# Performance work log

Measured on AMD Instinct MI355X. Metric: run time of the kernel, lower is better.

Reference implementation:

```python
import jax, jax.numpy as jnp
import numpy as np

N_NODES = 20000
N_EDGES = 640000
IN_DIM, HIDDEN, OUT_DIM = 128, 256, 64
EPS = 1e-12


def setup_inputs() -> dict:
    key = jax.random.key(0)
    ks = jax.random.split(key, 8)
    x = jax.random.normal(ks[0], (N_NODES, IN_DIM), dtype=jnp.float32)
    edge_src = jax.random.randint(ks[1], (N_EDGES,), 0, N_NODES, dtype=jnp.int32)
    edge_dst = jax.random.randint(ks[2], (N_EDGES,), 0, N_NODES, dtype=jnp.int32)
    s1 = 1.0 / np.sqrt(IN_DIM)
    s2 = 1.0 / np.sqrt(HIDDEN)
    W1 = jax.random.uniform(ks[3], (IN_DIM, HIDDEN), jnp.float32, -s1, s1)
    b1 = jax.random.uniform(ks[4], (HIDDEN,), jnp.float32, -s1, s1)
    W2 = jax.random.uniform(ks[5], (HIDDEN, OUT_DIM), jnp.float32, -s2, s2)
    b2 = jax.random.uniform(ks[6], (OUT_DIM,), jnp.float32, -s2, s2)
    return {"x": x, "edge_src": edge_src, "edge_dst": edge_dst,
            "W1": W1, "b1": b1, "W2": W2, "b2": b2}


def _agnn_layer(h, src, dst, n_nodes):
    # AGNN propagation with beta = 1 (non-trainable buffer in source module):
    # out_i = sum_j softmax_j(cos(h_i, h_j)) * h_j over neighbors j (incl. self-loop)
    hn = h * jax.lax.rsqrt(jnp.sum(h * h, axis=-1, keepdims=True) + EPS)
    logits = jnp.sum(hn[src] * hn[dst], axis=-1)            # [E] cosine similarity
    m = jax.ops.segment_max(logits, dst, num_segments=n_nodes)
    e = jnp.exp(logits - m[dst])
    z = jax.ops.segment_sum(e, dst, num_segments=n_nodes)
    alpha = e / z[dst]                                       # per-dst softmax
    return jax.ops.segment_sum(alpha[:, None] * h[src], dst, num_segments=n_nodes)


def reference(x, edge_src, edge_dst, W1, b1, W2, b2):
    n = x.shape[0]
    loop = jnp.arange(n, dtype=edge_src.dtype)
    src = jnp.concatenate([edge_src, loop])
    dst = jnp.concatenate([edge_dst, loop])
    h = jax.nn.relu(x @ W1 + b1)
    for _ in range(4):
        h = jax.nn.relu(_agnn_layer(h, src, dst, n))
    return h @ W2 + b2
```

## Files before the change

kernel.cpp:

```cpp
#include <hip/hip_runtime.h>

#define N_NODES 20000
#define N_EDGES 640000
#define E_TOT   (N_EDGES + N_NODES)
#define IN_DIM  128
#define HIDDEN  256
#define OUT_DIM 64
#define LOG2E 1.4426950408889634f
#define NSHARD 8

typedef __attribute__((ext_vector_type(2))) float f32x2;

__device__ __forceinline__ unsigned short f2bf(float f) {
    union { float f; unsigned int i; } x; x.f = f;
    unsigned int u = x.i;
    return (unsigned short)((u + 0x7fffu + ((u >> 16) & 1u)) >> 16);
}
__device__ __forceinline__ f32x2 up2(unsigned int p) {
    f32x2 r;
    r.x = __uint_as_float(p << 16);
    r.y = __uint_as_float(p & 0xffff0000u);
    return r;
}
__device__ __forceinline__ unsigned int pk2(float a, float b) {
    return (unsigned int)f2bf(a) | ((unsigned int)f2bf(b) << 16);
}


__global__ void zero_cnt8_kernel(int* __restrict__ cnt8) {
    int i = blockIdx.x * blockDim.x + threadIdx.x;
    if (i < NSHARD * N_NODES) cnt8[i] = 0;
}

__global__ void count_kernel(const int* __restrict__ edge_dst, int* __restrict__ cnt8) {
    int i = blockIdx.x * blockDim.x + threadIdx.x;
    if (i >= E_TOT) return;
    int shard = blockIdx.x & (NSHARD - 1);
    int d = (i < N_EDGES) ? edge_dst[i] : (i - N_EDGES);
    atomicAdd(&cnt8[shard * N_NODES + d], 1);
}

__global__ void sumdeg_kernel(const int* __restrict__ cnt8, int* __restrict__ deg) {
    int i = blockIdx.x * blockDim.x + threadIdx.x;
    if (i >= N_NODES) return;
    int s = 0;
#pragma unroll
    for (int s8 = 0; s8 < NSHARD; s8++) s += cnt8[s8 * N_NODES + i];
    deg[i] = s;
}

__global__ __launch_bounds__(1024) void scan1b_kernel(const int* __restrict__ deg,
                                                      int* __restrict__ indptr) {
    const int T = 1024;
    const int C = (N_NODES + T - 1) / T;
    __shared__ int sums[T];
    int t = threadIdx.x;
    int base = t * C;
    int local[C];
    int s = 0;
#pragma unroll
    for (int i = 0; i < C; i++) {
        int idx = base + i;
        int v = (idx < N_NODES) ? deg[idx] : 0;
        local[i] = s;
        s += v;
    }
    sums[t] = s;
    __syncthreads();
    for (int off = 1; off < T; off <<= 1) {
        int v = (t >= off) ? sums[t - off] : 0;
        __syncthreads();
        sums[t] += v;
        __syncthreads();
    }
    int prefix = (t == 0) ? 0 : sums[t - 1];
#pragma unroll
    for (int i = 0; i < C; i++) {
        int idx = base + i;
        if (idx < N_NODES) indptr[idx] = prefix + local[i];
    }
    if (t == T - 1) indptr[N_NODES] = prefix + s;
}

__global__ void cursor_kernel(const int* __restrict__ indptr, int* __restrict__ cnt8) {
    int i = blockIdx.x * blockDim.x + threadIdx.x;
    if (i >= N_NODES) return;
    int running = indptr[i];
#pragma unroll
    for (int s8 = 0; s8 < NSHARD; s8++) {
        int c = cnt8[s8 * N_NODES + i];
        cnt8[s8 * N_NODES + i] = running;
        running += c;
    }
}

__global__ void scatter_edges_kernel(const int* __restrict__ edge_src,
                                     const int* __restrict__ edge_dst,
                                     int* __restrict__ cnt8,
                                     int* __restrict__ ssrc) {
    int i = blockIdx.x * blockDim.x + threadIdx.x;
    if (i >= E_TOT) return;
    int shard = blockIdx.x & (NSHARD - 1);
    int d, s;
    if (i < N_EDGES) { d = edge_dst[i]; s = edge_src[i]; }
    else             { d = i - N_EDGES; s = d; }
    int pos = atomicAdd(&cnt8[shard * N_NODES + d], 1);
    ssrc[pos] = s;
}


__global__ __launch_bounds__(256) void gemm1_norm_kernel(const float* __restrict__ A,
                                                         const float* __restrict__ W,
                                                         const float* __restrict__ bias,
                                                         unsigned short* __restrict__ hnb,
                                                         float* __restrict__ r) {
    __shared__ float As[16][20];
    __shared__ float Bs[16][260];
    int t = threadIdx.x;
    int row = t >> 4;
    int cg  = t & 15;
    int grow = blockIdx.x * 16 + row;
    float4 acc0 = make_float4(0.f, 0.f, 0.f, 0.f);
    float4 acc1 = acc0, acc2 = acc0, acc3 = acc0;

    for (int k0 = 0; k0 < IN_DIM; k0 += 16) {
        {
            As[row][cg] = A[(long)grow * IN_DIM + k0 + cg];
        }
        {
            const float4* src = (const float4*)&W[(long)(k0 + row) * HIDDEN];
#pragma unroll
            for (int j = 0; j < 4; j++)
                *((float4*)&Bs[row][4 * cg + 64 * j]) = src[cg + 16 * j];
        }
        __syncthreads();
#pragma unroll
        for (int kk = 0; kk < 16; kk++) {
            float a = As[row][kk];
            float4 q0 = *((const float4*)&Bs[kk][4 * cg]);
            float4 q1 = *((const float4*)&Bs[kk][4 * cg + 64]);
            float4 q2 = *((const float4*)&Bs[kk][4 * cg + 128]);
            float4 q3 = *((const float4*)&Bs[kk][4 * cg + 192]);
            acc0.x += a * q0.x; acc0.y += a * q0.y; acc0.z += a * q0.z; acc0.w += a * q0.w;
            acc1.x += a * q1.x; acc1.y += a * q1.y; acc1.z += a * q1.z; acc1.w += a * q1.w;
            acc2.x += a * q2.x; acc2.y += a * q2.y; acc2.z += a * q2.z; acc2.w += a * q2.w;
            acc3.x += a * q3.x; acc3.y += a * q3.y; acc3.z += a * q3.z; acc3.w += a * q3.w;
        }
        __syncthreads();
    }

    float ss = 0.f;
    {
        float4 bv = *((const float4*)&bias[4 * cg]);
        acc0.x = fmaxf(acc0.x + bv.x, 0.f); acc0.y = fmaxf(acc0.y + bv.y, 0.f);
        acc0.z = fmaxf(acc0.z + bv.z, 0.f); acc0.w = fmaxf(acc0.w + bv.w, 0.f);
        ss += acc0.x * acc0.x + acc0.y * acc0.y + acc0.z * acc0.z + acc0.w * acc0.w;
    }
    {
        float4 bv = *((const float4*)&bias[4 * cg + 64]);
        acc1.x = fmaxf(acc1.x + bv.x, 0.f); acc1.y = fmaxf(acc1.y + bv.y, 0.f);
        acc1.z = fmaxf(acc1.z + bv.z, 0.f); acc1.w = fmaxf(acc1.w + bv.w, 0.f);
        ss += acc1.x * acc1.x + acc1.y * acc1.y + acc1.z * acc1.z + acc1.w * acc1.w;
    }
    {
        float4 bv = *((const float4*)&bias[4 * cg + 128]);
        acc2.x = fmaxf(acc2.x + bv.x, 0.f); acc2.y = fmaxf(acc2.y + bv.y, 0.f);
        acc2.z = fmaxf(acc2.z + bv.z, 0.f); acc2.w = fmaxf(acc2.w + bv.w, 0.f);
        ss += acc2.x * acc2.x + acc2.y * acc2.y + acc2.z * acc2.z + acc2.w * acc2.w;
    }
    {
        float4 bv = *((const float4*)&bias[4 * cg + 192]);
        acc3.x = fmaxf(acc3.x + bv.x, 0.f); acc3.y = fmaxf(acc3.y + bv.y, 0.f);
        acc3.z = fmaxf(acc3.z + bv.z, 0.f); acc3.w = fmaxf(acc3.w + bv.w, 0.f);
        ss += acc3.x * acc3.x + acc3.y * acc3.y + acc3.z * acc3.z + acc3.w * acc3.w;
    }
    ss += __shfl_xor(ss, 1);
    ss += __shfl_xor(ss, 2);
    ss += __shfl_xor(ss, 4);
    ss += __shfl_xor(ss, 8);
    float rr = sqrtf(ss + 1e-12f);
    float ir = 1.f / rr;
    uint2* dst = (uint2*)(hnb + (long)grow * HIDDEN);
    uint2 o;
    o.x = pk2(acc0.x * ir, acc0.y * ir); o.y = pk2(acc0.z * ir, acc0.w * ir);
    dst[cg]      = o;
    o.x = pk2(acc1.x * ir, acc1.y * ir); o.y = pk2(acc1.z * ir, acc1.w * ir);
    dst[cg + 16] = o;
    o.x = pk2(acc2.x * ir, acc2.y * ir); o.y = pk2(acc2.z * ir, acc2.w * ir);
    dst[cg + 32] = o;
    o.x = pk2(acc3.x * ir, acc3.y * ir); o.y = pk2(acc3.z * ir, acc3.w * ir);
    dst[cg + 48] = o;
    if (cg == 0) r[grow] = rr;
}


__global__ __launch_bounds__(256) void gemm_bias_act(const float* __restrict__ A,
                                                     const float* __restrict__ B,
                                                     const float* __restrict__ bias,
                                                     float* __restrict__ C,
                                                     int M, int Nn, int K, int relu) {
    __shared__ float As[16][65];
    __shared__ float Bs[16][65];
    int tid = threadIdx.x;
    int tx = tid & 15, ty = tid >> 4;
    int row0 = blockIdx.x * 64, col0 = blockIdx.y * 64;
    float acc[4][4] = {};
    for (int k0 = 0; k0 < K; k0 += 16) {
        {
            int r_ = tid >> 2;
            int kq = (tid & 3) * 4;
            int gr = row0 + r_;
            float4 a4 = make_float4(0.f, 0.f, 0.f, 0.f);
            if (gr < M) a4 = *(const float4*)&A[(long)gr * K + k0 + kq];
            As[kq + 0][r_] = a4.x; As[kq + 1][r_] = a4.y;
            As[kq + 2][r_] = a4.z; As[kq + 3][r_] = a4.w;
        }
        {
            int kr = tid >> 4;
            int cq = (tid & 15) * 4;
            float4 b4 = *(const float4*)&B[(long)(k0 + kr) * Nn + col0 + cq];
            Bs[kr][cq + 0] = b4.x; Bs[kr][cq + 1] = b4.y;
            Bs[kr][cq + 2] = b4.z; Bs[kr][cq + 3] = b4.w;
        }
        __syncthreads();
#pragma unroll
        for (int kk = 0; kk < 16; kk++) {
            float a[4], b[4];
#pragma unroll
            for (int i = 0; i < 4; i++) a[i] = As[kk][ty * 4 + i];
#pragma unroll
            for (int j = 0; j < 4; j++) b[j] = Bs[kk][tx * 4 + j];
#pragma unroll
            for (int i = 0; i < 4; i++)
#pragma unroll
                for (int j = 0; j < 4; j++) acc[i][j] += a[i] * b[j];
        }
        __syncthreads();
    }
#pragma unroll
    for (int i = 0; i < 4; i++) {
        int gr = row0 + ty * 4 + i;
        if (gr >= M) continue;
#pragma unroll
        for (int j = 0; j < 4; j++) {
            int gc = col0 + tx * 4 + j;
            float v = acc[i][j] + bias[gc];
            if (relu) v = fmaxf(v, 0.f);
            C[(long)gr * Nn + gc] = v;
        }
    }
}


__global__ __launch_bounds__(256) void agnn_kernel(const unsigned short* __restrict__ hnb,
                                                   const float* __restrict__ rin,
                                                   const int* __restrict__ indptr,
                                                   const int* __restrict__ ssrc,
                                                   unsigned short* __restrict__ hnout,
                                                   float* __restrict__ rout,
                                                   float* __restrict__ hout,
                                                   int write_hn) {
    int lane = threadIdx.x & 63;
    int wid  = threadIdx.x >> 6;
    int sub  = lane >> 4;
    int gl   = lane & 15;
    int node = blockIdx.x * 4 + wid;

    const uint4* tab4 = (const uint4*)hnb;
    long nb = (long)node * 32 + gl * 2;
    uint4 ha = tab4[nb], hb = tab4[nb + 1];
    f32x2 hd2[8];
    hd2[0] = up2(ha.x) * LOG2E; hd2[1] = up2(ha.y) * LOG2E;
    hd2[2] = up2(ha.z) * LOG2E; hd2[3] = up2(ha.w) * LOG2E;
    hd2[4] = up2(hb.x) * LOG2E; hd2[5] = up2(hb.y) * LOG2E;
    hd2[6] = up2(hb.z) * LOG2E; hd2[7] = up2(hb.w) * LOG2E;

    int beg = indptr[node], end = indptr[node + 1];
    int deg = end - beg;
    int qb  = deg >> 2, rem = deg & 3;
    int cnt = qb + (sub < rem ? 1 : 0);
    int eb  = beg + sub * qb + min(sub, rem);
    int nmax = qb + (rem ? 1 : 0);

    f32x2 acc[8];
#pragma unroll
    for (int p = 0; p < 8; p++) acc[p] = (f32x2)0.f;
    float z = 0.f;

    int s0 = ssrc[(cnt > 0) ? eb : beg];
    long b0 = (long)s0 * 32 + gl * 2;
    uint4 v0a = tab4[b0], v0b = tab4[b0 + 1];
    float r0 = rin[s0];
    uint4 v1a = v0a, v1b = v0b;
    float r1 = 0.f;
    int s2 = s0;
    if (cnt >= 2) {
        int s1 = ssrc[eb + 1];
        long b1 = (long)s1 * 32 + gl * 2;
        v1a = tab4[b1]; v1b = tab4[b1 + 1];
        r1 = rin[s1];
    }
    if (cnt >= 3) s2 = ssrc[eb + 2];

    for (int i = 0; i < nmax; i++) {
        uint4 ca = v0a, cb = v0b;
        float cr = r0;
        v0a = v1a; v0b = v1b; r0 = r1;
        if (i + 2 < cnt) {
            long b2 = (long)s2 * 32 + gl * 2;
            v1a = tab4[b2]; v1b = tab4[b2 + 1];
            r1 = rin[s2];
        }
        if (i + 3 < cnt) s2 = ssrc[eb + i + 3];

        f32x2 cf[8];
        cf[0] = up2(ca.x); cf[1] = up2(ca.y); cf[2] = up2(ca.z); cf[3] = up2(ca.w);
        cf[4] = up2(cb.x); cf[5] = up2(cb.y); cf[6] = up2(cb.z); cf[7] = up2(cb.w);
        f32x2 da = cf[0] * hd2[0];
        f32x2 db = cf[1] * hd2[1];
        da += cf[2] * hd2[2];  db += cf[3] * hd2[3];
        da += cf[4] * hd2[4];  db += cf[5] * hd2[5];
        da += cf[6] * hd2[6];  db += cf[7] * hd2[7];
        f32x2 d2 = da + db;
        float d = d2.x + d2.y;
        d += __shfl_xor(d, 1);
        d += __shfl_xor(d, 2);
        d += __shfl_xor(d, 4);
        d += __shfl_xor(d, 8);
        float w = (i < cnt) ? exp2f(d) : 0.f;
        z += w;
        float wr = w * cr;
#pragma unroll
        for (int p = 0; p < 8; p++) acc[p] += cf[p] * wr;
    }

    z += __shfl_xor(z, 16);
    z += __shfl_xor(z, 32);
#pragma unroll
    for (int p = 0; p < 8; p++) {
        acc[p].x += __shfl_xor(acc[p].x, 16);
        acc[p].y += __shfl_xor(acc[p].y, 16);
        acc[p].x += __shfl_xor(acc[p].x, 32);
        acc[p].y += __shfl_xor(acc[p].y, 32);
    }

    float inv = 1.f / z;
    f32x2 o[8];
#pragma unroll
    for (int p = 0; p < 8; p++) {
        f32x2 t = acc[p] * inv;
        t.x = fmaxf(t.x, 0.f);
        t.y = fmaxf(t.y, 0.f);
        o[p] = t;
    }

    if (write_hn) {
        float ss = 0.f;
#pragma unroll
        for (int p = 0; p < 8; p++) ss += o[p].x * o[p].x + o[p].y * o[p].y;
        ss += __shfl_xor(ss, 1);
        ss += __shfl_xor(ss, 2);
        ss += __shfl_xor(ss, 4);
        ss += __shfl_xor(ss, 8);
        float rr = sqrtf(ss + 1e-12f);
        float ir = 1.f / rr;
        if (sub == 0) {
            uint4 oa, ob;
            oa.x = pk2(o[0].x * ir, o[0].y * ir);
            oa.y = pk2(o[1].x * ir, o[1].y * ir);
            oa.z = pk2(o[2].x * ir, o[2].y * ir);
            oa.w = pk2(o[3].x * ir, o[3].y * ir);
            ob.x = pk2(o[4].x * ir, o[4].y * ir);
            ob.y = pk2(o[5].x * ir, o[5].y * ir);
            ob.z = pk2(o[6].x * ir, o[6].y * ir);
            ob.w = pk2(o[7].x * ir, o[7].y * ir);
            uint4* outt = (uint4*)hnout;
            outt[nb] = oa;
            outt[nb + 1] = ob;
            if (gl == 0) rout[node] = rr;
        }
    } else {
        if (sub == 0) {
            float4* ho = (float4*)(hout + (long)node * HIDDEN + gl * 16);
            ho[0] = make_float4(o[0].x, o[0].y, o[1].x, o[1].y);
            ho[1] = make_float4(o[2].x, o[2].y, o[3].x, o[3].y);
            ho[2] = make_float4(o[4].x, o[4].y, o[5].x, o[5].y);
            ho[3] = make_float4(o[6].x, o[6].y, o[7].x, o[7].y);
        }
    }
}


extern "C" void kernel_launch(void* const* d_in, const int* in_sizes, int n_in,
                              void* d_out, int out_size, void* d_ws, size_t ws_size,
                              hipStream_t stream) {
    const float* x  = (const float*)d_in[0];
    const int* esrc = (const int*)d_in[1];
    const int* edst = (const int*)d_in[2];
    const float* W1 = (const float*)d_in[3];
    const float* b1 = (const float*)d_in[4];
    const float* W2 = (const float*)d_in[5];
    const float* b2 = (const float*)d_in[6];
    float* out = (float*)d_out;

    char* ws = (char*)d_ws;
    float*          h0     = (float*)(ws);
    unsigned short* hnA    = (unsigned short*)(ws + 20480000);
    unsigned short* hnB    = (unsigned short*)(ws + 30720000);
    float*          rA     = (float*)(ws + 40960000);
    float*          rB     = (float*)(ws + 41040000);
    int*            indptr = (int*)  (ws + 41120000);
    int*            cnt8   = (int*)  (ws + 41200256);
    int*            ssrc   = (int*)  (ws + 41840256);
    int*            deg    = (int*)  (ws + 44480256);

    zero_cnt8_kernel<<<(NSHARD * N_NODES + 255) / 256, 256, 0, stream>>>(cnt8);
    count_kernel<<<(E_TOT + 255) / 256, 256, 0, stream>>>(edst, cnt8);
    sumdeg_kernel<<<(N_NODES + 255) / 256, 256, 0, stream>>>(cnt8, deg);
    scan1b_kernel<<<1, 1024, 0, stream>>>(deg, indptr);
    cursor_kernel<<<(N_NODES + 255) / 256, 256, 0, stream>>>(indptr, cnt8);
    scatter_edges_kernel<<<(E_TOT + 255) / 256, 256, 0, stream>>>(esrc, edst, cnt8, ssrc);

    gemm1_norm_kernel<<<N_NODES / 16, 256, 0, stream>>>(x, W1, b1, hnA, rA);

    int nblk = N_NODES / 4;
    agnn_kernel<<<nblk, 256, 0, stream>>>(hnA, rA, indptr, ssrc, hnB, rB, h0, 1);
    agnn_kernel<<<nblk, 256, 0, stream>>>(hnB, rB, indptr, ssrc, hnA, rA, h0, 1);
    agnn_kernel<<<nblk, 256, 0, stream>>>(hnA, rA, indptr, ssrc, hnB, rB, h0, 1);
    agnn_kernel<<<nblk, 256, 0, stream>>>(hnB, rB, indptr, ssrc, hnA, rA, h0, 0);

    dim3 g2((N_NODES + 63) / 64, OUT_DIM / 64);
    gemm_bias_act<<<g2, 256, 0, stream>>>(h0, W2, b2, out, N_NODES, OUT_DIM, HIDDEN, 0);
}
```

Baseline: 309.9 us.

## Fuse CSR construction kernels into one cooperative kernel with grid syncs

Replaces the six separate CSR-building launches (zero, count, degree sum, scan, cursor, scatter) with a single cooperative kernel that separates the phases with grid-wide syncs. The single-block scan is replaced by a two-level wave-shuffle scan over 1000 chunks of 20 nodes. This is meant to remove per-launch overhead and the serial single-block scan. In exchange it adds grid.sync costs and caps parallelism at 1024 blocks for the edge loops, and it requires all 1024 blocks to be co-resident.

```diff
diff --git a/kernel.cpp b/kernel.cpp
--- a/kernel.cpp
+++ b/kernel.cpp
@@ -1,4 +1,7 @@
 #include <hip/hip_runtime.h>
+#include <hip/hip_cooperative_groups.h>
+
+namespace cg = cooperative_groups;
 
 #define N_NODES 20000
 #define N_EDGES 640000
@@ -8,6 +11,8 @@
 #define OUT_DIM 64
 #define LOG2E 1.4426950408889634f
 #define NSHARD 8
+#define CSR_BLOCKS 1024
+#define CSR_THREADS 256
 
 typedef __attribute__((ext_vector_type(2))) float f32x2;
 
@@ -27,85 +32,108 @@
 }
 
 
-__global__ void zero_cnt8_kernel(int* __restrict__ cnt8) {
-    int i = blockIdx.x * blockDim.x + threadIdx.x;
-    if (i < NSHARD * N_NODES) cnt8[i] = 0;
-}
-
-__global__ void count_kernel(const int* __restrict__ edge_dst, int* __restrict__ cnt8) {
-    int i = blockIdx.x * blockDim.x + threadIdx.x;
-    if (i >= E_TOT) return;
-    int shard = blockIdx.x & (NSHARD - 1);
-    int d = (i < N_EDGES) ? edge_dst[i] : (i - N_EDGES);
-    atomicAdd(&cnt8[shard * N_NODES + d], 1);
-}
-
-__global__ void sumdeg_kernel(const int* __restrict__ cnt8, int* __restrict__ deg) {
-    int i = blockIdx.x * blockDim.x + threadIdx.x;
-    if (i >= N_NODES) return;
-    int s = 0;
-#pragma unroll
-    for (int s8 = 0; s8 < NSHARD; s8++) s += cnt8[s8 * N_NODES + i];
-    deg[i] = s;
-}
-
-__global__ __launch_bounds__(1024) void scan1b_kernel(const int* __restrict__ deg,
-                                                      int* __restrict__ indptr) {
-    const int T = 1024;
-    const int C = (N_NODES + T - 1) / T;
-    __shared__ int sums[T];
-    int t = threadIdx.x;
-    int base = t * C;
-    int local[C];
-    int s = 0;
-#pragma unroll
-    for (int i = 0; i < C; i++) {
-        int idx = base + i;
-        int v = (idx < N_NODES) ? deg[idx] : 0;
-        local[i] = s;
-        s += v;
-    }
-    sums[t] = s;
-    __syncthreads();
-    for (int off = 1; off < T; off <<= 1) {
-        int v = (t >= off) ? sums[t - off] : 0;
+__global__ __launch_bounds__(CSR_THREADS) void csr_coop_kernel(
+        const int* __restrict__ esrc, const int* __restrict__ edst,
+        int* __restrict__ cnt8, int* __restrict__ deg, int* __restrict__ indptr,
+        int* __restrict__ bsum, int* __restrict__ ssrc) {
+    cg::grid_group grid = cg::this_grid();
+    int bid = blockIdx.x, tid = threadIdx.x;
+    int gtid = bid * CSR_THREADS + tid;
+    const int GT = CSR_BLOCKS * CSR_THREADS;
+    int shard = bid & (NSHARD - 1);
+
+    for (int i = gtid; i < NSHARD * N_NODES; i += GT) cnt8[i] = 0;
+    grid.sync();
+
+    for (int i = gtid; i < E_TOT; i += GT) {
+        int d = (i < N_EDGES) ? edst[i] : (i - N_EDGES);
+        atomicAdd(&cnt8[shard * N_NODES + d], 1);
+    }
+    grid.sync();
+
+    for (int i = gtid; i < N_NODES; i += GT) {
+        int s = 0;
+#pragma unroll
+        for (int s8 = 0; s8 < NSHARD; s8++) s += cnt8[s8 * N_NODES + i];
+        deg[i] = s;
+    }
+    grid.sync();
+
+    if (bid < 1000 && tid < 32) {
+        int idx = bid * 20 + tid;
+        int v = (tid < 20) ? deg[idx] : 0;
+        int x = v;
+#pragma unroll
+        for (int off = 1; off < 32; off <<= 1) {
+            int y = __shfl_up(x, off);
+            if (tid >= off) x += y;
+        }
+        if (tid == 19) bsum[bid] = x;
+    }
+    grid.sync();
+
+    if (bid == 0) {
+        __shared__ int sm[CSR_THREADS];
+        int base = tid * 4;
+        int l0 = 0, l1 = 0, l2 = 0, l3 = 0;
+        if (base < 1000) {
+            l0 = bsum[base];
+            l1 = (base + 1 < 1000) ? bsum[base + 1] : 0;
+            l2 = (base + 2 < 1000) ? bsum[base + 2] : 0;
+            l3 = (base + 3 < 1000) ? bsum[base + 3] : 0;
+        }
+        int tot = l0 + l1 + l2 + l3;
+        sm[tid] = tot;
         __syncthreads();
-        sums[t] += v;
-        __syncthreads();
-    }
-    int prefix = (t == 0) ? 0 : sums[t - 1];
-#pragma unroll
-    for (int i = 0; i < C; i++) {
-        int idx = base + i;
-        if (idx < N_NODES) indptr[idx] = prefix + local[i];
-    }
-    if (t == T - 1) indptr[N_NODES] = prefix + s;
-}
-
-__global__ void cursor_kernel(const int* __restrict__ indptr, int* __restrict__ cnt8) {
-    int i = blockIdx.x * blockDim.x + threadIdx.x;
-    if (i >= N_NODES) return;
-    int running = indptr[i];
-#pragma unroll
-    for (int s8 = 0; s8 < NSHARD; s8++) {
-        int c = cnt8[s8 * N_NODES + i];
-        cnt8[s8 * N_NODES + i] = running;
-        running += c;
-    }
-}
-
-__global__ void scatter_edges_kernel(const int* __restrict__ edge_src,
-                                     const int* __restrict__ edge_dst,
-                                     int* __restrict__ cnt8,
-                                     int* __restrict__ ssrc) {
-    int i = blockIdx.x * blockDim.x + threadIdx.x;
-    if (i >= E_TOT) return;
-    int shard = blockIdx.x & (NSHARD - 1);
-    int d, s;
-    if (i < N_EDGES) { d = edge_dst[i]; s = edge_src[i]; }
-    else             { d = i - N_EDGES; s = d; }
-    int pos = atomicAdd(&cnt8[shard * N_NODES + d], 1);
-    ssrc[pos] = s;
+        for (int off = 1; off < CSR_THREADS; off <<= 1) {
+            int v = (tid >= off) ? sm[tid - off] : 0;
+            __syncthreads();
+            sm[tid] += v;
+            __syncthreads();
+        }
+        int pre = (tid == 0) ? 0 : sm[tid - 1];
+        if (base < 1000) {
+            bsum[base] = pre;
+            if (base + 1 < 1000) bsum[base + 1] = pre + l0;
+            if (base + 2 < 1000) bsum[base + 2] = pre + l0 + l1;
+            if (base + 3 < 1000) bsum[base + 3] = pre + l0 + l1 + l2;
+        }
+        if (tid == CSR_THREADS - 1) bsum[1000] = sm[CSR_THREADS - 1];
+    }
+    grid.sync();
+
+    if (bid < 1000 && tid < 32) {
+        int idx = bid * 20 + tid;
+        int v = (tid < 20) ? deg[idx] : 0;
+        int x = v;
+#pragma unroll
+        for (int off = 1; off < 32; off <<= 1) {
+            int y = __shfl_up(x, off);
+            if (tid >= off) x += y;
+        }
+        if (tid < 20) indptr[idx] = bsum[bid] + x - v;
+    }
+    if (gtid == 0) indptr[N_NODES] = bsum[1000];
+    grid.sync();
+
+    for (int i = gtid; i < N_NODES; i += GT) {
+        int running = indptr[i];
+#pragma unroll
+        for (int s8 = 0; s8 < NSHARD; s8++) {
+            int c = cnt8[s8 * N_NODES + i];
+            cnt8[s8 * N_NODES + i] = running;
+            running += c;
+        }
+    }
+    grid.sync();
+
+    for (int i = gtid; i < E_TOT; i += GT) {
+        int d, s;
+        if (i < N_EDGES) { d = edst[i]; s = esrc[i]; }
+        else             { d = i - N_EDGES; s = d; }
+        int pos = atomicAdd(&cnt8[shard * N_NODES + d], 1);
+        ssrc[pos] = s;
+    }
 }
 
 
@@ -124,9 +152,7 @@
     float4 acc1 = acc0, acc2 = acc0, acc3 = acc0;
 
     for (int k0 = 0; k0 < IN_DIM; k0 += 16) {
-        {
-            As[row][cg] = A[(long)grow * IN_DIM + k0 + cg];
-        }
+        As[row][cg] = A[(long)grow * IN_DIM + k0 + cg];
         {
             const float4* src = (const float4*)&W[(long)(k0 + row) * HIDDEN];
 #pragma unroll
@@ -413,13 +439,15 @@
     int*            cnt8   = (int*)  (ws + 41200256);
     int*            ssrc   = (int*)  (ws + 41840256);
     int*            deg    = (int*)  (ws + 44480256);
-
-    zero_cnt8_kernel<<<(NSHARD * N_NODES + 255) / 256, 256, 0, stream>>>(cnt8);
-    count_kernel<<<(E_TOT + 255) / 256, 256, 0, stream>>>(edst, cnt8);
-    sumdeg_kernel<<<(N_NODES + 255) / 256, 256, 0, stream>>>(cnt8, deg);
-    scan1b_kernel<<<1, 1024, 0, stream>>>(deg, indptr);
-    cursor_kernel<<<(N_NODES + 255) / 256, 256, 0, stream>>>(indptr, cnt8);
-    scatter_edges_kernel<<<(E_TOT + 255) / 256, 256, 0, stream>>>(esrc, edst, cnt8, ssrc);
+    int*            bsum   = (int*)  (ws + 44560256);
+
+    {
+        void* args[] = { (void*)&esrc, (void*)&edst, (void*)&cnt8, (void*)&deg,
+                         (void*)&indptr, (void*)&bsum, (void*)&ssrc };
+        hipLaunchCooperativeKernel((void*)csr_coop_kernel,
+                                   dim3(CSR_BLOCKS), dim3(CSR_THREADS),
+                                   args, 0, stream);
+    }
 
     gemm1_norm_kernel<<<N_NODES / 16, 256, 0, stream>>>(x, W1, b1, hnA, rA);
 
```

Measured after the change: 1.045 ms. 237% more time.

## Partially sort CSR neighbor lists by source-node octant for gather locality

Applied to the files above, without the earlier changes.

Edge sharding for the CSR build now uses (source octant × XCD) buckets, 64 in all, instead of 8 XCD buckets. Each destination's neighbor list therefore comes out roughly grouped by source-node range. The aim is better cache locality when the AGNN layers gather neighbor feature rows. In exchange, the count buffer grows eightfold, and the zero, sumdeg and cursor passes each touch 64 shards per node.

```diff
diff --git a/kernel.cpp b/kernel.cpp
--- a/kernel.cpp
+++ b/kernel.cpp
@@ -7,7 +7,9 @@
 #define HIDDEN  256
 #define OUT_DIM 64
 #define LOG2E 1.4426950408889634f
-#define NSHARD 8
+#define NOCT   8
+#define NXCD   8
+#define NSH    (NOCT * NXCD)
 
 typedef __attribute__((ext_vector_type(2))) float f32x2;
 
@@ -27,25 +29,30 @@
 }
 
 
-__global__ void zero_cnt8_kernel(int* __restrict__ cnt8) {
+__global__ void zero_cnt_kernel(int* __restrict__ cnt) {
     int i = blockIdx.x * blockDim.x + threadIdx.x;
-    if (i < NSHARD * N_NODES) cnt8[i] = 0;
-}
-
-__global__ void count_kernel(const int* __restrict__ edge_dst, int* __restrict__ cnt8) {
+    if (i < NSH * N_NODES) cnt[i] = 0;
+}
+
+__global__ void count_kernel(const int* __restrict__ edge_src,
+                             const int* __restrict__ edge_dst,
+                             int* __restrict__ cnt) {
     int i = blockIdx.x * blockDim.x + threadIdx.x;
     if (i >= E_TOT) return;
-    int shard = blockIdx.x & (NSHARD - 1);
-    int d = (i < N_EDGES) ? edge_dst[i] : (i - N_EDGES);
-    atomicAdd(&cnt8[shard * N_NODES + d], 1);
-}
-
-__global__ void sumdeg_kernel(const int* __restrict__ cnt8, int* __restrict__ deg) {
+    int xcd = blockIdx.x & (NXCD - 1);
+    int d, s;
+    if (i < N_EDGES) { d = edge_dst[i]; s = edge_src[i]; }
+    else             { d = i - N_EDGES; s = d; }
+    int shard = (s / 2500) * NXCD + xcd;
+    atomicAdd(&cnt[shard * N_NODES + d], 1);
+}
+
+__global__ void sumdeg_kernel(const int* __restrict__ cnt, int* __restrict__ deg) {
     int i = blockIdx.x * blockDim.x + threadIdx.x;
     if (i >= N_NODES) return;
     int s = 0;
 #pragma unroll
-    for (int s8 = 0; s8 < NSHARD; s8++) s += cnt8[s8 * N_NODES + i];
+    for (int s8 = 0; s8 < NSH; s8++) s += cnt[s8 * N_NODES + i];
     deg[i] = s;
 }
 
@@ -82,29 +89,30 @@
     if (t == T - 1) indptr[N_NODES] = prefix + s;
 }
 
-__global__ void cursor_kernel(const int* __restrict__ indptr, int* __restrict__ cnt8) {
+__global__ void cursor_kernel(const int* __restrict__ indptr, int* __restrict__ cnt) {
     int i = blockIdx.x * blockDim.x + threadIdx.x;
     if (i >= N_NODES) return;
     int running = indptr[i];
 #pragma unroll
-    for (int s8 = 0; s8 < NSHARD; s8++) {
-        int c = cnt8[s8 * N_NODES + i];
-        cnt8[s8 * N_NODES + i] = running;
+    for (int s8 = 0; s8 < NSH; s8++) {
+        int c = cnt[s8 * N_NODES + i];
+        cnt[s8 * N_NODES + i] = running;
         running += c;
     }
 }
 
 __global__ void scatter_edges_kernel(const int* __restrict__ edge_src,
                                      const int* __restrict__ edge_dst,
-                                     int* __restrict__ cnt8,
+                                     int* __restrict__ cnt,
                                      int* __restrict__ ssrc) {
     int i = blockIdx.x * blockDim.x + threadIdx.x;
     if (i >= E_TOT) return;
-    int shard = blockIdx.x & (NSHARD - 1);
+    int xcd = blockIdx.x & (NXCD - 1);
     int d, s;
     if (i < N_EDGES) { d = edge_dst[i]; s = edge_src[i]; }
     else             { d = i - N_EDGES; s = d; }
-    int pos = atomicAdd(&cnt8[shard * N_NODES + d], 1);
+    int shard = (s / 2500) * NXCD + xcd;
+    int pos = atomicAdd(&cnt[shard * N_NODES + d], 1);
     ssrc[pos] = s;
 }
 
@@ -124,9 +132,7 @@
     float4 acc1 = acc0, acc2 = acc0, acc3 = acc0;
 
     for (int k0 = 0; k0 < IN_DIM; k0 += 16) {
-        {
-            As[row][cg] = A[(long)grow * IN_DIM + k0 + cg];
-        }
+        As[row][cg] = A[(long)grow * IN_DIM + k0 + cg];
         {
             const float4* src = (const float4*)&W[(long)(k0 + row) * HIDDEN];
 #pragma unroll
@@ -410,16 +416,16 @@
     float*          rA     = (float*)(ws + 40960000);
     float*          rB     = (float*)(ws + 41040000);
     int*            indptr = (int*)  (ws + 41120000);
-    int*            cnt8   = (int*)  (ws + 41200256);
-    int*            ssrc   = (int*)  (ws + 41840256);
-    int*            deg    = (int*)  (ws + 44480256);
-
-    zero_cnt8_kernel<<<(NSHARD * N_NODES + 255) / 256, 256, 0, stream>>>(cnt8);
-    count_kernel<<<(E_TOT + 255) / 256, 256, 0, stream>>>(edst, cnt8);
-    sumdeg_kernel<<<(N_NODES + 255) / 256, 256, 0, stream>>>(cnt8, deg);
+    int*            cnt    = (int*)  (ws + 41200256);
+    int*            ssrc   = (int*)  (ws + 46320256);
+    int*            deg    = (int*)  (ws + 48960256);
+
+    zero_cnt_kernel<<<(NSH * N_NODES + 255) / 256, 256, 0, stream>>>(cnt);
+    count_kernel<<<(E_TOT + 255) / 256, 256, 0, stream>>>(esrc, edst, cnt);
+    sumdeg_kernel<<<(N_NODES + 255) / 256, 256, 0, stream>>>(cnt, deg);
     scan1b_kernel<<<1, 1024, 0, stream>>>(deg, indptr);
-    cursor_kernel<<<(N_NODES + 255) / 256, 256, 0, stream>>>(indptr, cnt8);
-    scatter_edges_kernel<<<(E_TOT + 255) / 256, 256, 0, stream>>>(esrc, edst, cnt8, ssrc);
+    cursor_kernel<<<(N_NODES + 255) / 256, 256, 0, stream>>>(indptr, cnt);
+    scatter_edges_kernel<<<(E_TOT + 255) / 256, 256, 0, stream>>>(esrc, edst, cnt, ssrc);
 
     gemm1_norm_kernel<<<N_NODES / 16, 256, 0, stream>>>(x, W1, b1, hnA, rA);
 
```

New measurement: 329.8 us. 6.4% more time.

## Schedule AGNN nodes in descending-degree order via counting-sort permutation

Applied to the files above, without the earlier changes.

Builds a degree histogram during CSR construction, scans it, and writes a node permutation sorted by descending in-degree. Each AGNN wave then processes nodes through this permutation, so waves within a block have similar degrees and heavy nodes start first, reducing tail imbalance. It adds histogram atomics, a second scan in the single-block kernel and one indirect load per wave. Because the degrees are near-uniform random, the balancing gain may be small, and nodes handled by neighbouring waves are no longer adjacent in memory.

```diff
diff --git a/kernel.cpp b/kernel.cpp
--- a/kernel.cpp
+++ b/kernel.cpp
@@ -8,6 +8,7 @@
 #define OUT_DIM 64
 #define LOG2E 1.4426950408889634f
 #define NSHARD 8
+#define NBIN 1024
 
 typedef __attribute__((ext_vector_type(2))) float f32x2;
 
@@ -27,9 +28,10 @@
 }
 
 
-__global__ void zero_cnt8_kernel(int* __restrict__ cnt8) {
+__global__ void zero_cnt8_kernel(int* __restrict__ cnt8, int* __restrict__ hist8) {
     int i = blockIdx.x * blockDim.x + threadIdx.x;
     if (i < NSHARD * N_NODES) cnt8[i] = 0;
+    if (i < NSHARD * NBIN) hist8[i] = 0;
 }
 
 __global__ void count_kernel(const int* __restrict__ edge_dst, int* __restrict__ cnt8) {
@@ -40,17 +42,22 @@
     atomicAdd(&cnt8[shard * N_NODES + d], 1);
 }
 
-__global__ void sumdeg_kernel(const int* __restrict__ cnt8, int* __restrict__ deg) {
+__global__ void sumdeg_kernel(const int* __restrict__ cnt8, int* __restrict__ deg,
+                              int* __restrict__ hist8) {
     int i = blockIdx.x * blockDim.x + threadIdx.x;
     if (i >= N_NODES) return;
+    int shard = blockIdx.x & (NSHARD - 1);
     int s = 0;
 #pragma unroll
     for (int s8 = 0; s8 < NSHARD; s8++) s += cnt8[s8 * N_NODES + i];
     deg[i] = s;
+    int key = (NBIN - 1) - ((s > NBIN - 1) ? (NBIN - 1) : s);
+    atomicAdd(&hist8[shard * NBIN + key], 1);
 }
 
 __global__ __launch_bounds__(1024) void scan1b_kernel(const int* __restrict__ deg,
-                                                      int* __restrict__ indptr) {
+                                                      int* __restrict__ indptr,
+                                                      int* __restrict__ hist8) {
     const int T = 1024;
     const int C = (N_NODES + T - 1) / T;
     __shared__ int sums[T];
@@ -80,9 +87,30 @@
         if (idx < N_NODES) indptr[idx] = prefix + local[i];
     }
     if (t == T - 1) indptr[N_NODES] = prefix + s;
-}
-
-__global__ void cursor_kernel(const int* __restrict__ indptr, int* __restrict__ cnt8) {
+    __syncthreads();
+    int h[NSHARD];
+    int tot = 0;
+#pragma unroll
+    for (int s8 = 0; s8 < NSHARD; s8++) { h[s8] = hist8[s8 * NBIN + t]; tot += h[s8]; }
+    sums[t] = tot;
+    __syncthreads();
+    for (int off = 1; off < T; off <<= 1) {
+        int v = (t >= off) ? sums[t - off] : 0;
+        __syncthreads();
+        sums[t] += v;
+        __syncthreads();
+    }
+    int running = sums[t] - tot;
+#pragma unroll
+    for (int s8 = 0; s8 < NSHARD; s8++) {
+        hist8[s8 * NBIN + t] = running;
+        running += h[s8];
+    }
+}
+
+__global__ void cursor_kernel(const int* __restrict__ indptr, int* __restrict__ cnt8,
+                              const int* __restrict__ deg, int* __restrict__ hist8,
+                              int* __restrict__ perm) {
     int i = blockIdx.x * blockDim.x + threadIdx.x;
     if (i >= N_NODES) return;
     int running = indptr[i];
@@ -92,6 +120,11 @@
         cnt8[s8 * N_NODES + i] = running;
         running += c;
     }
+    int shard = blockIdx.x & (NSHARD - 1);
+    int dv = deg[i];
+    int key = (NBIN - 1) - ((dv > NBIN - 1) ? (NBIN - 1) : dv);
+    int pos = atomicAdd(&hist8[shard * NBIN + key], 1);
+    perm[pos] = i;
 }
 
 __global__ void scatter_edges_kernel(const int* __restrict__ edge_src,
@@ -124,9 +157,7 @@
     float4 acc1 = acc0, acc2 = acc0, acc3 = acc0;
 
     for (int k0 = 0; k0 < IN_DIM; k0 += 16) {
-        {
-            As[row][cg] = A[(long)grow * IN_DIM + k0 + cg];
-        }
+        As[row][cg] = A[(long)grow * IN_DIM + k0 + cg];
         {
             const float4* src = (const float4*)&W[(long)(k0 + row) * HIDDEN];
 #pragma unroll
@@ -256,6 +287,7 @@
                                                    const float* __restrict__ rin,
                                                    const int* __restrict__ indptr,
                                                    const int* __restrict__ ssrc,
+                                                   const int* __restrict__ perm,
                                                    unsigned short* __restrict__ hnout,
                                                    float* __restrict__ rout,
                                                    float* __restrict__ hout,
@@ -264,7 +296,7 @@
     int wid  = threadIdx.x >> 6;
     int sub  = lane >> 4;
     int gl   = lane & 15;
-    int node = blockIdx.x * 4 + wid;
+    int node = perm[blockIdx.x * 4 + wid];
 
     const uint4* tab4 = (const uint4*)hnb;
     long nb = (long)node * 32 + gl * 2;
@@ -413,21 +445,23 @@
     int*            cnt8   = (int*)  (ws + 41200256);
     int*            ssrc   = (int*)  (ws + 41840256);
     int*            deg    = (int*)  (ws + 44480256);
-
-    zero_cnt8_kernel<<<(NSHARD * N_NODES + 255) / 256, 256, 0, stream>>>(cnt8);
+    int*            hist8  = (int*)  (ws + 44560256);
+    int*            perm   = (int*)  (ws + 44593024);
+
+    zero_cnt8_kernel<<<(NSHARD * N_NODES + 255) / 256, 256, 0, stream>>>(cnt8, hist8);
     count_kernel<<<(E_TOT + 255) / 256, 256, 0, stream>>>(edst, cnt8);
-    sumdeg_kernel<<<(N_NODES + 255) / 256, 256, 0, stream>>>(cnt8, deg);
-    scan1b_kernel<<<1, 1024, 0, stream>>>(deg, indptr);
-    cursor_kernel<<<(N_NODES + 255) / 256, 256, 0, stream>>>(indptr, cnt8);
+    sumdeg_kernel<<<(N_NODES + 255) / 256, 256, 0, stream>>>(cnt8, deg, hist8);
+    scan1b_kernel<<<1, 1024, 0, stream>>>(deg, indptr, hist8);
+    cursor_kernel<<<(N_NODES + 255) / 256, 256, 0, stream>>>(indptr, cnt8, deg, hist8, perm);
     scatter_edges_kernel<<<(E_TOT + 255) / 256, 256, 0, stream>>>(esrc, edst, cnt8, ssrc);
 
     gemm1_norm_kernel<<<N_NODES / 16, 256, 0, stream>>>(x, W1, b1, hnA, rA);
 
     int nblk = N_NODES / 4;
-    agnn_kernel<<<nblk, 256, 0, stream>>>(hnA, rA, indptr, ssrc, hnB, rB, h0, 1);
-    agnn_kernel<<<nblk, 256, 0, stream>>>(hnB, rB, indptr, ssrc, hnA, rA, h0, 1);
-    agnn_kernel<<<nblk, 256, 0, stream>>>(hnA, rA, indptr, ssrc, hnB, rB, h0, 1);
-    agnn_kernel<<<nblk, 256, 0, stream>>>(hnB, rB, indptr, ssrc, hnA, rA, h0, 0);
+    agnn_kernel<<<nblk, 256, 0, stream>>>(hnA, rA, indptr, ssrc, perm, hnB, rB, h0, 1);
+    agnn_kernel<<<nblk, 256, 0, stream>>>(hnB, rB, indptr, ssrc, perm, hnA, rA, h0, 1);
+    agnn_kernel<<<nblk, 256, 0, stream>>>(hnA, rA, indptr, ssrc, perm, hnB, rB, h0, 1);
+    agnn_kernel<<<nblk, 256, 0, stream>>>(hnB, rB, indptr, ssrc, perm, hnA, rA, h0, 0);
 
     dim3 g2((N_NODES + 63) / 64, OUT_DIM / 64);
     gemm_bias_act<<<g2, 256, 0, stream>>>(h0, W2, b2, out, N_NODES, OUT_DIM, HIDDEN, 0);
```

Result: slower. 324.9 us (+4.8%).
